# Optimization experiments

Measured on AMD Instinct MI355X. Metric: run time of the kernel, lower is better.

## Reference

```python
import jax, jax.numpy as jnp
import numpy as np

N = 50000
E = 800000
NUM_GRAPHS = 128
X_IN, HID, EDGE_DIM = 64, 64, 16


def setup_inputs() -> dict:
    key = jax.random.key(0)
    ks = jax.random.split(key, 9)
    s = 0.05
    inp = {
        'x': jax.random.normal(ks[0], (N, X_IN), jnp.float32),
        'edge_index': jax.random.randint(ks[1], (2, E), 0, N, dtype=jnp.int32),
        'edge_attr': jax.random.normal(ks[2], (E, EDGE_DIM), jnp.float32),
        'batch': jnp.sort(jax.random.randint(ks[3], (N,), 0, NUM_GRAPHS, dtype=jnp.int32)),
        'w_fc1': jax.random.normal(ks[4], (EDGE_DIM, 1), jnp.float32) * s,
        'b_fc1': jnp.zeros((1,), jnp.float32),
    }
    dims = [(X_IN, HID), (HID, HID * 2), (HID * 2, HID)]
    for i, (din, dout) in enumerate(dims):
        k1, k2, k3 = jax.random.split(ks[5 + i], 3)
        inp[f'w1_{i}'] = jax.random.normal(k1, (din, dout), jnp.float32) * s
        inp[f'b1_{i}'] = jnp.zeros((dout,), jnp.float32)
        inp[f'w2_{i}'] = jax.random.normal(k2, (din, dout), jnp.float32) * s
        inp[f'w3_{i}'] = jax.random.normal(k3, (din, dout), jnp.float32) * s
        inp[f'b3_{i}'] = jnp.zeros((dout,), jnp.float32)
    return inp


def leconv(x, src, dst, ew, w1, b1, w2, w3, b3):
    # PyG LEConv: out_i = lin3(x_i) + sum_{j->i} e_ji * (lin1(x_j) - lin2(x_i))
    a = x @ w1 + b1          # lin1 (bias=True)   [N, out]
    b = x @ w2               # lin2 (bias=False)  [N, out]
    msg = ew[:, None] * (a[src] - b[dst])          # [E, out]
    agg = jax.ops.segment_sum(msg, dst, num_segments=N)
    return agg + x @ w3 + b3  # lin3 (bias=True)


def reference(x, edge_index, edge_attr, batch,
              w_fc1, b_fc1,
              w1_0, b1_0, w2_0, w3_0, b3_0,
              w1_1, b1_1, w2_1, w3_1, b3_1,
              w1_2, b1_2, w2_2, w3_2, b3_2):
    src, dst = edge_index[0], edge_index[1]
    ew = (edge_attr @ w_fc1 + b_fc1)[:, 0]         # fc1(edge_attr).squeeze(-1) -> [E]
    h = jax.nn.elu(leconv(x, src, dst, ew, w1_0, b1_0, w2_0, w3_0, b3_0))
    h = jax.nn.elu(leconv(h, src, dst, ew, w1_1, b1_1, w2_1, w3_1, b3_1))
    h = jax.nn.elu(leconv(h, src, dst, ew, w1_2, b1_2, w2_2, w3_2, b3_2))
    # global max pool over nodes of each graph -> [NUM_GRAPHS, HID]
    return jax.ops.segment_max(h, batch, num_segments=NUM_GRAPHS)
```

## Files before the change

### kernel.cpp

```cpp
#include <hip/hip_runtime.h>
#include <math.h>

#define N_NODES 50000
#define N_EDGES 800000
#define NUM_GRAPHS_ 128
#define SCAN_NB 98
#define NPASS 8
#define NODES_PER_PASS 6250
#define HCHUNKS 128
#define EDGES_PER_CHUNK 6250
#define HWORDS 12500

typedef unsigned short u16;
typedef unsigned int u32;
typedef __attribute__((ext_vector_type(8))) short bf16x8;
typedef __attribute__((ext_vector_type(4))) float f32x4;

__device__ __forceinline__ float elu_f(float v) {
    return v > 0.f ? v : (__expf(v) - 1.f);
}
__device__ __forceinline__ u16 f2bf(float f) {
    u32 u = __float_as_uint(f);
    u += 0x7FFFu + ((u >> 16) & 1u);
    return (u16)(u >> 16);
}
__device__ __forceinline__ float bf2f(u16 h) {
    return __uint_as_float(((u32)h) << 16);
}
__device__ __forceinline__ void bfpair(u32 v, float& lo, float& hi) {
    lo = __uint_as_float(v << 16);
    hi = __uint_as_float(v & 0xFFFF0000u);
}
__device__ __forceinline__ u32 packbf(float lo, float hi) {
    return (u32)f2bf(lo) | ((u32)f2bf(hi) << 16);
}

__global__ void conv_x_kernel(const float* __restrict__ x, u16* __restrict__ xb) {
    int g = blockIdx.x * blockDim.x + threadIdx.x;
    float4 v = ((const float4*)x)[g];
    uint2 o;
    o.x = packbf(v.x, v.y);
    o.y = packbf(v.z, v.w);
    ((uint2*)xb)[g] = o;
}

__global__ void ew_kernel(const float* __restrict__ edge_attr,
                          const float* __restrict__ w_fc1,
                          const float* __restrict__ b_fc1,
                          const int* __restrict__ edge_index,
                          float* __restrict__ ew,
                          u16* __restrict__ dst16) {
    int e = blockIdx.x * blockDim.x + threadIdx.x;
    if (e >= N_EDGES) return;
    const float4* ea = (const float4*)(edge_attr + (size_t)e * 16);
    const float4* wf = (const float4*)w_fc1;
    float acc = b_fc1[0];
#pragma unroll
    for (int i = 0; i < 4; i++) {
        float4 a = ea[i], w = wf[i];
        acc += a.x * w.x + a.y * w.y + a.z * w.z + a.w * w.w;
    }
    ew[e] = acc;
    dst16[e] = (u16)edge_index[N_EDGES + e];
}

__global__ __launch_bounds__(256) void deg_hist_kernel(const u16* __restrict__ dst16,
                                                       u32* __restrict__ partial) {
    __shared__ u32 bins[HWORDS];
    const int c = blockIdx.x >> 1;
    const int p = blockIdx.x & 1;
    const int t = threadIdx.x;
    for (int i = t; i < HWORDS; i += 256) bins[i] = 0;
    __syncthreads();
    const int base = c * EDGES_PER_CHUNK;
    const int nlo = p * 25000;
    for (int i = t; i < EDGES_PER_CHUNK; i += 256) {
        const int b = (int)dst16[base + i] - nlo;
        if ((unsigned)b < 25000u)
            atomicAdd(&bins[b >> 1], 1u << ((b & 1) * 16));
    }
    __syncthreads();
    u32* outp = partial + (size_t)blockIdx.x * HWORDS;
    for (int i = t; i < HWORDS; i += 256) outp[i] = bins[i];
}

__global__ __launch_bounds__(256) void scan_chunks_kernel(const u32* __restrict__ partial,
                                                          u32* __restrict__ prefpack,
                                                          u32* __restrict__ degpack) {
    const int g = blockIdx.x * 256 + threadIdx.x;
    if (g >= 25000) return;
    const int p = (g >= HWORDS) ? 1 : 0;
    const int wh = g - p * HWORDS;
    u32 runlo = 0, runhi = 0;
    for (int c = 0; c < HCHUNKS; c++) {
        prefpack[(size_t)c * 25000 + g] = runlo | (runhi << 16);
        u32 v = partial[(size_t)((c << 1) + p) * HWORDS + wh];
        runlo += v & 0xFFFFu;
        runhi += v >> 16;
    }
    degpack[g] = runlo | (runhi << 16);
}

__global__ __launch_bounds__(256) void scan1_kernel(const u32* __restrict__ degpack,
                                                    int* __restrict__ rowptr,
                                                    int* __restrict__ blk_sums) {
    __shared__ int sh[256];
    const int t = threadIdx.x;
    const int base = blockIdx.x * 512;
    const int i0 = base + 2 * t, i1 = i0 + 1;
    int d0 = 0, d1 = 0;
    if (i0 < N_NODES) {
        u32 v = degpack[i0 >> 1];
        d0 = (int)(v & 0xFFFFu);
        d1 = (int)(v >> 16);
    }
    const int pair = d0 + d1;
    int v = pair;
    sh[t] = v;
    __syncthreads();
#pragma unroll
    for (int off = 1; off < 256; off <<= 1) {
        int add = (t >= off) ? sh[t - off] : 0;
        __syncthreads();
        v += add;
        sh[t] = v;
        __syncthreads();
    }
    const int excl = v - pair;
    if (i0 < N_NODES) rowptr[i0] = excl;
    if (i1 < N_NODES) rowptr[i1] = excl + d0;
    if (t == 255) blk_sums[blockIdx.x] = v;
}

__global__ __launch_bounds__(128) void scan2_kernel(const int* __restrict__ blk_sums,
                                                    int* __restrict__ blk_offs,
                                                    int* __restrict__ rowptr) {
    __shared__ int sh[128];
    const int t = threadIdx.x;
    const int orig = (t < SCAN_NB) ? blk_sums[t] : 0;
    int v = orig;
    sh[t] = v;
    __syncthreads();
#pragma unroll
    for (int off = 1; off < 128; off <<= 1) {
        int add = (t >= off) ? sh[t - off] : 0;
        __syncthreads();
        v += add;
        sh[t] = v;
        __syncthreads();
    }
    if (t < SCAN_NB) blk_offs[t] = v - orig;
    if (t == 127) rowptr[N_NODES] = v;
}

__global__ void scan3_kernel(int* __restrict__ rowptr,
                             const int* __restrict__ blk_offs) {
    int i = blockIdx.x * blockDim.x + threadIdx.x;
    if (i >= N_NODES) return;
    rowptr[i] += blk_offs[i >> 9];
}

__global__ __launch_bounds__(256) void place_kernel(const int* __restrict__ edge_index,
                                                    const float* __restrict__ ew,
                                                    const u16* __restrict__ dst16,
                                                    const int* __restrict__ rowptr,
                                                    const u32* __restrict__ prefpack,
                                                    int2* __restrict__ csr) {
    __shared__ int lcur[NODES_PER_PASS];
    const int pass = blockIdx.x & (NPASS - 1);
    const int c = blockIdx.x >> 3;
    const int lo = pass * NODES_PER_PASS;
    const int t = threadIdx.x;
    for (int i = t; i < NODES_PER_PASS; i += 256) lcur[i] = 0;
    __syncthreads();
    const int base = c * EDGES_PER_CHUNK;
    for (int i = t; i < EDGES_PER_CHUNK; i += 256) {
        const int e = base + i;
        const int d = (int)dst16[e];
        const int dl = d - lo;
        if ((unsigned)dl < (unsigned)NODES_PER_PASS) {
            u32 pw = prefpack[(size_t)c * 25000 + (d >> 1)];
            int pref = (int)((pw >> ((d & 1) * 16)) & 0xFFFFu);
            int lpos = atomicAdd(&lcur[dl], 1);
            int2 ent;
            ent.x = edge_index[e];
            ent.y = __float_as_int(ew[e]);
            csr[rowptr[d] + pref + lpos] = ent;
        }
    }
}

template <int DIN, bool WRITE_C>
__global__ __launch_bounds__(256) void gather_kernel(
    const u16* __restrict__ xb, const int* __restrict__ rowptr,
    const int2* __restrict__ csr, u16* __restrict__ sb,
    u16* __restrict__ chb, float* __restrict__ c) {
    constexpr int CG = DIN / 4;
    constexpr int EG = 64 / CG;
    const int gid = blockIdx.x * 256 + threadIdx.x;
    const int node = gid >> 6;
    if (node >= N_NODES) return;
    const int lane = threadIdx.x & 63;
    const int cg = lane & (CG - 1);
    const int eg = lane / CG;
    const int beg = rowptr[node];
    const int end = rowptr[node + 1];
    const uint2* x2 = (const uint2*)xb;

    float a0 = 0.f, a1 = 0.f, a2 = 0.f, a3 = 0.f;
    float b0 = 0.f, b1 = 0.f, b2 = 0.f, b3 = 0.f;
    float wsum = 0.f;

    int p = beg + eg;
    for (; p + EG < end; p += 2 * EG) {
        int2 e0 = csr[p];
        int2 e1 = csr[p + EG];
        float w0 = __int_as_float(e0.y);
        float w1 = __int_as_float(e1.y);
        uint2 v0 = x2[(size_t)e0.x * CG + cg];
        uint2 v1 = x2[(size_t)e1.x * CG + cg];
        float f0, f1, f2, f3, g0, g1, g2, g3;
        bfpair(v0.x, f0, f1); bfpair(v0.y, f2, f3);
        bfpair(v1.x, g0, g1); bfpair(v1.y, g2, g3);
        a0 += w0 * f0; a1 += w0 * f1; a2 += w0 * f2; a3 += w0 * f3;
        b0 += w1 * g0; b1 += w1 * g1; b2 += w1 * g2; b3 += w1 * g3;
        wsum += w0 + w1;
    }
    if (p < end) {
        int2 e0 = csr[p];
        float w0 = __int_as_float(e0.y);
        uint2 v0 = x2[(size_t)e0.x * CG + cg];
        float f0, f1, f2, f3;
        bfpair(v0.x, f0, f1); bfpair(v0.y, f2, f3);
        a0 += w0 * f0; a1 += w0 * f1; a2 += w0 * f2; a3 += w0 * f3;
        wsum += w0;
    }
    a0 += b0; a1 += b1; a2 += b2; a3 += b3;

#pragma unroll
    for (int off = 32; off >= CG; off >>= 1) {
        a0 += __shfl_xor(a0, off);
        a1 += __shfl_xor(a1, off);
        a2 += __shfl_xor(a2, off);
        a3 += __shfl_xor(a3, off);
        wsum += __shfl_xor(wsum, off);
    }

    if (lane < CG) {
        uint2 so;
        so.x = packbf(a0, a1);
        so.y = packbf(a2, a3);
        ((uint2*)sb)[(size_t)node * CG + cg] = so;
        const float cn = WRITE_C ? wsum : c[node];
        uint2 hv = x2[(size_t)node * CG + cg];
        float h0, h1, h2, h3;
        bfpair(hv.x, h0, h1); bfpair(hv.y, h2, h3);
        uint2 co;
        co.x = packbf(cn * h0, cn * h1);
        co.y = packbf(cn * h2, cn * h3);
        ((uint2*)chb)[(size_t)node * CG + cg] = co;
    }
    if (WRITE_C && lane == 0) c[node] = wsum;
}

__global__ void pack_w_kernel(const float* __restrict__ w3_0, const float* __restrict__ w1_0, const float* __restrict__ w2_0,
                              const float* __restrict__ w3_1, const float* __restrict__ w1_1, const float* __restrict__ w2_1,
                              const float* __restrict__ w3_2, const float* __restrict__ w1_2, const float* __restrict__ w2_2,
                              u16* __restrict__ bp0, u16* __restrict__ bp1, u16* __restrict__ bp2) {
    int t = blockIdx.x * blockDim.x + threadIdx.x;
    if (t >= 7680) return;
    u16 buf[8];
    if (t < 4608) {
        int DIN, DOUT, lid;
        const float *w3, *w1, *w2;
        u16* bp;
        if (t < 1536) { DIN = 64; DOUT = 64;  lid = t;        w3 = w3_0; w1 = w1_0; w2 = w2_0; bp = bp0; }
        else          { DIN = 64; DOUT = 128; lid = t - 1536; w3 = w3_1; w1 = w1_1; w2 = w2_1; bp = bp1; }
        const int NT = DOUT / 16;
        const int lane = lid & 63;
        const int fragid = lid >> 6;
        const int chunk = fragid / NT;
        const int ntile = fragid % NT;
        const int n = ntile * 16 + (lane & 15);
        const int kbase = chunk * 32 + (lane >> 4) * 8;
#pragma unroll
        for (int j = 0; j < 8; j++) {
            int k = kbase + j;
            int region = k / DIN;
            int kk = k - region * DIN;
            float v = (region == 0) ? w3[kk * DOUT + n]
                    : (region == 1) ? w1[kk * DOUT + n]
                                    : -w2[kk * DOUT + n];
            buf[j] = f2bf(v);
        }
        *(bf16x8*)(bp + ((size_t)lid << 3)) = *(bf16x8*)buf;
    } else {
        const int lid = t - 4608;
        const int NT = 12;
        const int lane = lid & 63;
        const int fragid = lid >> 6;
        const int chunk = fragid / NT;
        const int ntile = fragid % NT;
        const int n = ntile * 16 + (lane & 15);
        const int kbase = chunk * 32 + (lane >> 4) * 8;
#pragma unroll
        for (int j = 0; j < 8; j++) {
            int k = kbase + j;
            float v = (n < 64)  ? w3_2[k * 64 + n]
                    : (n < 128) ? -w2_2[k * 64 + (n - 64)]
                                : w1_2[k * 64 + (n - 128)];
            buf[j] = f2bf(v);
        }
        *(bf16x8*)(bp2 + ((size_t)lid << 3)) = *(bf16x8*)buf;
    }
}

template <int DIN, int DOUT>
__global__ __launch_bounds__(256) void gemm_mfma(
    const u16* __restrict__ hb, const u16* __restrict__ sb,
    const u16* __restrict__ chb, const u16* __restrict__ Bp,
    const float* __restrict__ cvec, const float* __restrict__ bias1,
    const float* __restrict__ bias3, u16* __restrict__ outp) {
    constexpr int CH = DIN / 32;
    constexpr int CHUNKS = 3 * CH;
    constexpr int NT = DOUT / 16;
    const int tid = threadIdx.x;
    const int wv = tid >> 6;
    const int lane = tid & 63;
    const int l15 = lane & 15;
    const int q = lane >> 4;
    const int mhalf = wv & 1;
    const int nhalf = wv >> 1;
    const int row_base = blockIdx.x * 64 + mhalf * 32;
    const int nt0 = blockIdx.y * 4 + nhalf * 2;

    const int r0 = min(row_base + l15, N_NODES - 1);
    const int r1 = min(row_base + 16 + l15, N_NODES - 1);
    const int qo = q * 8;

    f32x4 acc00 = {0.f, 0.f, 0.f, 0.f};
    f32x4 acc01 = {0.f, 0.f, 0.f, 0.f};
    f32x4 acc10 = {0.f, 0.f, 0.f, 0.f};
    f32x4 acc11 = {0.f, 0.f, 0.f, 0.f};

#pragma unroll
    for (int chunk = 0; chunk < CHUNKS; chunk++) {
        const int region = chunk / CH;
        const int koff = (chunk - region * CH) * 32 + qo;
        const u16* A = (region == 0) ? hb : (region == 1) ? sb : chb;
        bf16x8 a0 = *(const bf16x8*)(A + (size_t)r0 * DIN + koff);
        bf16x8 a1 = *(const bf16x8*)(A + (size_t)r1 * DIN + koff);
        const u16* bp = Bp + (((size_t)(chunk * NT + nt0) * 64 + lane) << 3);
        bf16x8 bf0 = *(const bf16x8*)bp;
        bf16x8 bf1 = *(const bf16x8*)(bp + 64 * 8);
        acc00 = __builtin_amdgcn_mfma_f32_16x16x32_bf16(a0, bf0, acc00, 0, 0, 0);
        acc01 = __builtin_amdgcn_mfma_f32_16x16x32_bf16(a0, bf1, acc01, 0, 0, 0);
        acc10 = __builtin_amdgcn_mfma_f32_16x16x32_bf16(a1, bf0, acc10, 0, 0, 0);
        acc11 = __builtin_amdgcn_mfma_f32_16x16x32_bf16(a1, bf1, acc11, 0, 0, 0);
    }

#pragma unroll
    for (int ni = 0; ni < 2; ni++) {
        const int col = (nt0 + ni) * 16 + l15;
        const float B3 = bias3[col];
        const float B1 = bias1[col];
        const f32x4 am0 = ni ? acc01 : acc00;
        const f32x4 am1 = ni ? acc11 : acc10;
#pragma unroll
        for (int mi = 0; mi < 2; mi++) {
            const f32x4 av = mi ? am1 : am0;
#pragma unroll
            for (int reg = 0; reg < 4; reg++) {
                const int row = row_base + mi * 16 + q * 4 + reg;
                if (row < N_NODES) {
                    const float cv = cvec[row];
                    const float val = av[reg] + B3 + cv * B1;
                    outp[(size_t)row * DOUT + col] = f2bf(elu_f(val));
                }
            }
        }
    }
}

__global__ __launch_bounds__(256) void gemm_wide_kernel(
    const u16* __restrict__ hb, const u16* __restrict__ Bp,
    u16* __restrict__ zuy) {
    constexpr int NT = 12;
    const int tid = threadIdx.x;
    const int wv = tid >> 6;
    const int lane = tid & 63;
    const int l15 = lane & 15;
    const int q = lane >> 4;
    const int row_base = blockIdx.x * 64 + (wv & 1) * 32;
    const int nt0 = blockIdx.y * 4 + (wv >> 1) * 2;

    const int r0 = min(row_base + l15, N_NODES - 1);
    const int r1 = min(row_base + 16 + l15, N_NODES - 1);
    const int qo = q * 8;

    f32x4 acc00 = {0.f, 0.f, 0.f, 0.f};
    f32x4 acc01 = {0.f, 0.f, 0.f, 0.f};
    f32x4 acc10 = {0.f, 0.f, 0.f, 0.f};
    f32x4 acc11 = {0.f, 0.f, 0.f, 0.f};

#pragma unroll
    for (int chunk = 0; chunk < 4; chunk++) {
        const int koff = chunk * 32 + qo;
        bf16x8 a0 = *(const bf16x8*)(hb + (size_t)r0 * 128 + koff);
        bf16x8 a1 = *(const bf16x8*)(hb + (size_t)r1 * 128 + koff);
        const u16* bp = Bp + (((size_t)(chunk * NT + nt0) * 64 + lane) << 3);
        bf16x8 bf0 = *(const bf16x8*)bp;
        bf16x8 bf1 = *(const bf16x8*)(bp + 64 * 8);
        acc00 = __builtin_amdgcn_mfma_f32_16x16x32_bf16(a0, bf0, acc00, 0, 0, 0);
        acc01 = __builtin_amdgcn_mfma_f32_16x16x32_bf16(a0, bf1, acc01, 0, 0, 0);
        acc10 = __builtin_amdgcn_mfma_f32_16x16x32_bf16(a1, bf0, acc10, 0, 0, 0);
        acc11 = __builtin_amdgcn_mfma_f32_16x16x32_bf16(a1, bf1, acc11, 0, 0, 0);
    }

#pragma unroll
    for (int ni = 0; ni < 2; ni++) {
        const int col = (nt0 + ni) * 16 + l15;
        const f32x4 am0 = ni ? acc01 : acc00;
        const f32x4 am1 = ni ? acc11 : acc10;
#pragma unroll
        for (int mi = 0; mi < 2; mi++) {
            const f32x4 av = mi ? am1 : am0;
#pragma unroll
            for (int reg = 0; reg < 4; reg++) {
                const int row = row_base + mi * 16 + q * 4 + reg;
                if (row < N_NODES)
                    zuy[(size_t)row * 192 + col] = f2bf(av[reg]);
            }
        }
    }
}

__global__ __launch_bounds__(256) void gather2_kernel(
    const u16* __restrict__ zuy, const int* __restrict__ rowptr,
    const int2* __restrict__ csr, const float* __restrict__ c,
    const float* __restrict__ bias1, const float* __restrict__ bias3,
    u16* __restrict__ h3) {
    constexpr int CG = 16, EG = 4;
    const int gid = blockIdx.x * 256 + threadIdx.x;
    const int node = gid >> 6;
    if (node >= N_NODES) return;
    const int lane = threadIdx.x & 63;
    const int cg = lane & (CG - 1);
    const int eg = lane >> 4;
    const int beg = rowptr[node];
    const int end = rowptr[node + 1];

    float a0 = 0.f, a1 = 0.f, a2 = 0.f, a3 = 0.f;
    float b0 = 0.f, b1 = 0.f, b2 = 0.f, b3 = 0.f;

    int p = beg + eg;
    for (; p + EG < end; p += 2 * EG) {
        int2 e0 = csr[p];
        int2 e1 = csr[p + EG];
        float w0 = __int_as_float(e0.y);
        float w1 = __int_as_float(e1.y);
        uint2 v0 = ((const uint2*)(zuy + (size_t)e0.x * 192 + 128))[cg];
        uint2 v1 = ((const uint2*)(zuy + (size_t)e1.x * 192 + 128))[cg];
        float f0, f1, f2, f3, g0, g1, g2, g3;
        bfpair(v0.x, f0, f1); bfpair(v0.y, f2, f3);
        bfpair(v1.x, g0, g1); bfpair(v1.y, g2, g3);
        a0 += w0 * f0; a1 += w0 * f1; a2 += w0 * f2; a3 += w0 * f3;
        b0 += w1 * g0; b1 += w1 * g1; b2 += w1 * g2; b3 += w1 * g3;
    }
    if (p < end) {
        int2 e0 = csr[p];
        float w0 = __int_as_float(e0.y);
        uint2 v0 = ((const uint2*)(zuy + (size_t)e0.x * 192 + 128))[cg];
        float f0, f1, f2, f3;
        bfpair(v0.x, f0, f1); bfpair(v0.y, f2, f3);
        a0 += w0 * f0; a1 += w0 * f1; a2 += w0 * f2; a3 += w0 * f3;
    }
    a0 += b0; a1 += b1; a2 += b2; a3 += b3;

#pragma unroll
    for (int off = 32; off >= CG; off >>= 1) {
        a0 += __shfl_xor(a0, off);
        a1 += __shfl_xor(a1, off);
        a2 += __shfl_xor(a2, off);
        a3 += __shfl_xor(a3, off);
    }

    if (lane < CG) {
        const float cn = c[node];
        const u16* zr = zuy + (size_t)node * 192;
        uint2 zv = ((const uint2*)zr)[cg];
        uint2 uv = ((const uint2*)(zr + 64))[cg];
        float z0, z1, z2, z3, u0, u1, u2, u3;
        bfpair(zv.x, z0, z1); bfpair(zv.y, z2, z3);
        bfpair(uv.x, u0, u1); bfpair(uv.y, u2, u3);
        const float4 b3v = *(const float4*)(bias3 + cg * 4);
        const float4 b1v = *(const float4*)(bias1 + cg * 4);
        float o0 = elu_f(z0 + cn * u0 + a0 + b3v.x + cn * b1v.x);
        float o1 = elu_f(z1 + cn * u1 + a1 + b3v.y + cn * b1v.y);
        float o2 = elu_f(z2 + cn * u2 + a2 + b3v.z + cn * b1v.z);
        float o3 = elu_f(z3 + cn * u3 + a3 + b3v.w + cn * b1v.w);
        uint2 o;
        o.x = packbf(o0, o1);
        o.y = packbf(o2, o3);
        ((uint2*)h3)[(size_t)node * CG + cg] = o;
    }
}

__global__ void pool_kernel(const u16* __restrict__ h,
                            const int* __restrict__ batch,
                            float* __restrict__ out) {
    const int g = blockIdx.x;
    const int tid = threadIdx.x;
    int lo = 0, hi = N_NODES;
    while (lo < hi) { int mid = (lo + hi) >> 1; if (batch[mid] < g) lo = mid + 1; else hi = mid; }
    const int beg = lo;
    lo = beg; hi = N_NODES;
    while (lo < hi) { int mid = (lo + hi) >> 1; if (batch[mid] < g + 1) lo = mid + 1; else hi = mid; }
    const int end = lo;

    __shared__ float red[256];
    const int col = tid & 63;
    const int rg = tid >> 6;
    float m = -3.0e38f;
    for (int r = beg + rg; r < end; r += 4) m = fmaxf(m, bf2f(h[(size_t)r * 64 + col]));
    red[tid] = m;
    __syncthreads();
    if (tid < 64) {
        m = fmaxf(fmaxf(red[tid], red[tid + 64]), fmaxf(red[tid + 128], red[tid + 192]));
        out[g * 64 + tid] = m;
    }
}

extern "C" void kernel_launch(void* const* d_in, const int* in_sizes, int n_in,
                              void* d_out, int out_size, void* d_ws, size_t ws_size,
                              hipStream_t stream) {
    const float* x = (const float*)d_in[0];
    const int* ei = (const int*)d_in[1];
    const float* ea = (const float*)d_in[2];
    const int* batch = (const int*)d_in[3];
    const float* wfc = (const float*)d_in[4];
    const float* bfc = (const float*)d_in[5];
    const float* w1_0 = (const float*)d_in[6];
    const float* b1_0 = (const float*)d_in[7];
    const float* w2_0 = (const float*)d_in[8];
    const float* w3_0 = (const float*)d_in[9];
    const float* b3_0 = (const float*)d_in[10];
    const float* w1_1 = (const float*)d_in[11];
    const float* b1_1 = (const float*)d_in[12];
    const float* w2_1 = (const float*)d_in[13];
    const float* w3_1 = (const float*)d_in[14];
    const float* b3_1 = (const float*)d_in[15];
    const float* w1_2 = (const float*)d_in[16];
    const float* b1_2 = (const float*)d_in[17];
    const float* w2_2 = (const float*)d_in[18];
    const float* w3_2 = (const float*)d_in[19];
    const float* b3_2 = (const float*)d_in[20];
    float* out = (float*)d_out;

    char* ws = (char*)d_ws;
    float* ew      = (float*)(ws);
    float* c       = (float*)(ws + 3200000);
    int*   rowptr  = (int*)  (ws + 3800000);
    int2*  csr     = (int2*) (ws + 4000128);
    u16*   xb      = (u16*)  (ws + 10400128);
    u16*   sb      = (u16*)  (ws + 16800128);
    u16*   chb     = (u16*)  (ws + 29600128);
    u16*   h1      = (u16*)  (ws + 42400128);
    u16*   h2      = (u16*)  (ws + 48800128);
    u16*   h3      = (u16*)  (ws + 61600128);
    u16*   bp0     = (u16*)  (ws + 68000128);
    u16*   bp1     = (u16*)  (ws + 68024704);
    u16*   bp2     = (u16*)  (ws + 68073856);
    int* blk_sums  = (int*)  (ws + 68123008);
    int* blk_offs  = (int*)  (ws + 68123520);
    u16* dst16   = chb;
    u32* degpack = (u32*)(ws + 31600128);
    u32* partial = (u32*)sb;
    u32* prefpack = (u32*)h2;
    u16* zuy     = sb;

    conv_x_kernel<<<3125, 256, 0, stream>>>(x, xb);
    ew_kernel<<<(N_EDGES + 255) / 256, 256, 0, stream>>>(ea, wfc, bfc, ei, ew, dst16);
    pack_w_kernel<<<30, 256, 0, stream>>>(w3_0, w1_0, w2_0, w3_1, w1_1, w2_1,
                                          w3_2, w1_2, w2_2, bp0, bp1, bp2);
    deg_hist_kernel<<<HCHUNKS * 2, 256, 0, stream>>>(dst16, partial);
    scan_chunks_kernel<<<98, 256, 0, stream>>>(partial, prefpack, degpack);
    scan1_kernel<<<SCAN_NB, 256, 0, stream>>>(degpack, rowptr, blk_sums);
    scan2_kernel<<<1, 128, 0, stream>>>(blk_sums, blk_offs, rowptr);
    scan3_kernel<<<(N_NODES + 255) / 256, 256, 0, stream>>>(rowptr, blk_offs);
    place_kernel<<<HCHUNKS * NPASS, 256, 0, stream>>>(ei, ew, dst16, rowptr, prefpack, csr);

    const int RB = (N_NODES + 63) / 64;
    const int GBLK = (N_NODES * 64 + 255) / 256;

    gather_kernel<64, true><<<GBLK, 256, 0, stream>>>(xb, rowptr, csr, sb, chb, c);
    gemm_mfma<64, 64><<<dim3(RB, 1), 256, 0, stream>>>(xb, sb, chb, bp0, c, b1_0, b3_0, h1);

    gather_kernel<64, false><<<GBLK, 256, 0, stream>>>(h1, rowptr, csr, sb, chb, c);
    gemm_mfma<64, 128><<<dim3(RB, 2), 256, 0, stream>>>(h1, sb, chb, bp1, c, b1_1, b3_1, h2);

    gemm_wide_kernel<<<dim3(RB, 3), 256, 0, stream>>>(h2, bp2, zuy);
    gather2_kernel<<<GBLK, 256, 0, stream>>>(zuy, rowptr, csr, c, b1_2, b3_2, h3);

    pool_kernel<<<NUM_GRAPHS_, 256, 0, stream>>>(h3, batch, out);
}
```

Before: 349.7 us.

## Pack CSR entries to 32 bits, widen gather loads, merge prep kernels

Compresses each CSR entry from an int2 (src index, fp32 weight) to one u32 holding a 16-bit source index and a bf16 edge weight. This halves CSR traffic in the three gather passes. The gathers now use 8 lanes per row with 16-byte loads and 8 edges in flight. The x conversion, edge-weight and weight-packing kernels are fused into one launch, and histogram chunks go from 128 to 64. Rounding the edge weights to bf16 adds precision loss, and the 16-bit source index only works because N is at most 65535.

Measured after the change: 352.0 us. No clear change (+0.7%).

```diff
diff --git a/kernel.cpp b/kernel.cpp
--- a/kernel.cpp
+++ b/kernel.cpp
@@ -7,8 +7,8 @@
 #define SCAN_NB 98
 #define NPASS 8
 #define NODES_PER_PASS 6250
-#define HCHUNKS 128
-#define EDGES_PER_CHUNK 6250
+#define HCHUNKS 64
+#define EDGES_PER_CHUNK 12500
 #define HWORDS 12500
 
 typedef unsigned short u16;
@@ -34,34 +34,88 @@
 __device__ __forceinline__ u32 packbf(float lo, float hi) {
     return (u32)f2bf(lo) | ((u32)f2bf(hi) << 16);
 }
-
-__global__ void conv_x_kernel(const float* __restrict__ x, u16* __restrict__ xb) {
-    int g = blockIdx.x * blockDim.x + threadIdx.x;
-    float4 v = ((const float4*)x)[g];
-    uint2 o;
-    o.x = packbf(v.x, v.y);
-    o.y = packbf(v.z, v.w);
-    ((uint2*)xb)[g] = o;
-}
-
-__global__ void ew_kernel(const float* __restrict__ edge_attr,
-                          const float* __restrict__ w_fc1,
-                          const float* __restrict__ b_fc1,
-                          const int* __restrict__ edge_index,
-                          float* __restrict__ ew,
-                          u16* __restrict__ dst16) {
-    int e = blockIdx.x * blockDim.x + threadIdx.x;
-    if (e >= N_EDGES) return;
-    const float4* ea = (const float4*)(edge_attr + (size_t)e * 16);
-    const float4* wf = (const float4*)w_fc1;
-    float acc = b_fc1[0];
-#pragma unroll
-    for (int i = 0; i < 4; i++) {
-        float4 a = ea[i], w = wf[i];
-        acc += a.x * w.x + a.y * w.y + a.z * w.z + a.w * w.w;
-    }
-    ew[e] = acc;
-    dst16[e] = (u16)edge_index[N_EDGES + e];
+__device__ __forceinline__ void unpack8(uint4 v, float* f) {
+    bfpair(v.x, f[0], f[1]); bfpair(v.y, f[2], f[3]);
+    bfpair(v.z, f[4], f[5]); bfpair(v.w, f[6], f[7]);
+}
+
+__global__ __launch_bounds__(256) void prep_kernel(
+    const float* __restrict__ x, u16* __restrict__ xb,
+    const float* __restrict__ edge_attr, const float* __restrict__ w_fc1,
+    const float* __restrict__ b_fc1, const int* __restrict__ edge_index,
+    float* __restrict__ ew, u16* __restrict__ dst16,
+    const float* __restrict__ w3_0, const float* __restrict__ w1_0, const float* __restrict__ w2_0,
+    const float* __restrict__ w3_1, const float* __restrict__ w1_1, const float* __restrict__ w2_1,
+    const float* __restrict__ w3_2, const float* __restrict__ w1_2, const float* __restrict__ w2_2,
+    u16* __restrict__ bp0, u16* __restrict__ bp1, u16* __restrict__ bp2) {
+    const int b = blockIdx.x;
+    if (b < 3125) {
+        int g = b * 256 + threadIdx.x;
+        float4 v = ((const float4*)x)[g];
+        uint2 o;
+        o.x = packbf(v.x, v.y);
+        o.y = packbf(v.z, v.w);
+        ((uint2*)xb)[g] = o;
+    } else if (b < 6250) {
+        int e = (b - 3125) * 256 + threadIdx.x;
+        const float4* ea = (const float4*)(edge_attr + (size_t)e * 16);
+        const float4* wf = (const float4*)w_fc1;
+        float acc = b_fc1[0];
+#pragma unroll
+        for (int i = 0; i < 4; i++) {
+            float4 a = ea[i], w = wf[i];
+            acc += a.x * w.x + a.y * w.y + a.z * w.z + a.w * w.w;
+        }
+        ew[e] = acc;
+        dst16[e] = (u16)edge_index[N_EDGES + e];
+    } else {
+        int t = (b - 6250) * 256 + threadIdx.x;
+        if (t >= 7680) return;
+        u16 buf[8];
+        if (t < 4608) {
+            int DIN, DOUT, lid;
+            const float *w3, *w1, *w2;
+            u16* bp;
+            if (t < 1536) { DIN = 64; DOUT = 64;  lid = t;        w3 = w3_0; w1 = w1_0; w2 = w2_0; bp = bp0; }
+            else          { DIN = 64; DOUT = 128; lid = t - 1536; w3 = w3_1; w1 = w1_1; w2 = w2_1; bp = bp1; }
+            const int NT = DOUT / 16;
+            const int lane = lid & 63;
+            const int fragid = lid >> 6;
+            const int chunk = fragid / NT;
+            const int ntile = fragid % NT;
+            const int n = ntile * 16 + (lane & 15);
+            const int kbase = chunk * 32 + (lane >> 4) * 8;
+#pragma unroll
+            for (int j = 0; j < 8; j++) {
+                int k = kbase + j;
+                int region = k / DIN;
+                int kk = k - region * DIN;
+                float v = (region == 0) ? w3[kk * DOUT + n]
+                        : (region == 1) ? w1[kk * DOUT + n]
+                                        : -w2[kk * DOUT + n];
+                buf[j] = f2bf(v);
+            }
+            *(bf16x8*)(bp + ((size_t)lid << 3)) = *(bf16x8*)buf;
+        } else {
+            const int lid = t - 4608;
+            const int NT = 12;
+            const int lane = lid & 63;
+            const int fragid = lid >> 6;
+            const int chunk = fragid / NT;
+            const int ntile = fragid % NT;
+            const int n = ntile * 16 + (lane & 15);
+            const int kbase = chunk * 32 + (lane >> 4) * 8;
+#pragma unroll
+            for (int j = 0; j < 8; j++) {
+                int k = kbase + j;
+                float v = (n < 64)  ? w3_2[k * 64 + n]
+                        : (n < 128) ? -w2_2[k * 64 + (n - 64)]
+                                    : w1_2[k * 64 + (n - 128)];
+                buf[j] = f2bf(v);
+            }
+            *(bf16x8*)(bp2 + ((size_t)lid << 3)) = *(bf16x8*)buf;
+        }
+    }
 }
 
 __global__ __launch_bounds__(256) void deg_hist_kernel(const u16* __restrict__ dst16,
@@ -165,7 +219,7 @@
                                                     const u16* __restrict__ dst16,
                                                     const int* __restrict__ rowptr,
                                                     const u32* __restrict__ prefpack,
-                                                    int2* __restrict__ csr) {
+                                                    u32* __restrict__ csr) {
     __shared__ int lcur[NODES_PER_PASS];
     const int pass = blockIdx.x & (NPASS - 1);
     const int c = blockIdx.x >> 3;
@@ -182,137 +236,85 @@
             u32 pw = prefpack[(size_t)c * 25000 + (d >> 1)];
             int pref = (int)((pw >> ((d & 1) * 16)) & 0xFFFFu);
             int lpos = atomicAdd(&lcur[dl], 1);
-            int2 ent;
-            ent.x = edge_index[e];
-            ent.y = __float_as_int(ew[e]);
+            u32 ent = (u32)(u16)edge_index[e] | ((u32)f2bf(ew[e]) << 16);
             csr[rowptr[d] + pref + lpos] = ent;
         }
     }
 }
 
-template <int DIN, bool WRITE_C>
+template <bool WRITE_C>
 __global__ __launch_bounds__(256) void gather_kernel(
     const u16* __restrict__ xb, const int* __restrict__ rowptr,
-    const int2* __restrict__ csr, u16* __restrict__ sb,
+    const u32* __restrict__ csr, u16* __restrict__ sb,
     u16* __restrict__ chb, float* __restrict__ c) {
-    constexpr int CG = DIN / 4;
-    constexpr int EG = 64 / CG;
+    constexpr int CG = 8, EG = 8;
     const int gid = blockIdx.x * 256 + threadIdx.x;
     const int node = gid >> 6;
     if (node >= N_NODES) return;
     const int lane = threadIdx.x & 63;
     const int cg = lane & (CG - 1);
-    const int eg = lane / CG;
+    const int eg = lane >> 3;
     const int beg = rowptr[node];
     const int end = rowptr[node + 1];
-    const uint2* x2 = (const uint2*)xb;
-
-    float a0 = 0.f, a1 = 0.f, a2 = 0.f, a3 = 0.f;
-    float b0 = 0.f, b1 = 0.f, b2 = 0.f, b3 = 0.f;
+    const uint4* x4 = (const uint4*)xb;
+
+    float a[8] = {}, b[8] = {};
     float wsum = 0.f;
 
     int p = beg + eg;
     for (; p + EG < end; p += 2 * EG) {
-        int2 e0 = csr[p];
-        int2 e1 = csr[p + EG];
-        float w0 = __int_as_float(e0.y);
-        float w1 = __int_as_float(e1.y);
-        uint2 v0 = x2[(size_t)e0.x * CG + cg];
-        uint2 v1 = x2[(size_t)e1.x * CG + cg];
-        float f0, f1, f2, f3, g0, g1, g2, g3;
-        bfpair(v0.x, f0, f1); bfpair(v0.y, f2, f3);
-        bfpair(v1.x, g0, g1); bfpair(v1.y, g2, g3);
-        a0 += w0 * f0; a1 += w0 * f1; a2 += w0 * f2; a3 += w0 * f3;
-        b0 += w1 * g0; b1 += w1 * g1; b2 += w1 * g2; b3 += w1 * g3;
+        u32 e0 = csr[p];
+        u32 e1 = csr[p + EG];
+        float w0 = bf2f((u16)(e0 >> 16));
+        float w1 = bf2f((u16)(e1 >> 16));
+        uint4 v0 = x4[(size_t)(e0 & 0xFFFFu) * CG + cg];
+        uint4 v1 = x4[(size_t)(e1 & 0xFFFFu) * CG + cg];
+        float f[8], g[8];
+        unpack8(v0, f);
+        unpack8(v1, g);
+#pragma unroll
+        for (int j = 0; j < 8; j++) { a[j] += w0 * f[j]; b[j] += w1 * g[j]; }
         wsum += w0 + w1;
     }
     if (p < end) {
-        int2 e0 = csr[p];
-        float w0 = __int_as_float(e0.y);
-        uint2 v0 = x2[(size_t)e0.x * CG + cg];
-        float f0, f1, f2, f3;
-        bfpair(v0.x, f0, f1); bfpair(v0.y, f2, f3);
-        a0 += w0 * f0; a1 += w0 * f1; a2 += w0 * f2; a3 += w0 * f3;
+        u32 e0 = csr[p];
+        float w0 = bf2f((u16)(e0 >> 16));
+        uint4 v0 = x4[(size_t)(e0 & 0xFFFFu) * CG + cg];
+        float f[8];
+        unpack8(v0, f);
+#pragma unroll
+        for (int j = 0; j < 8; j++) a[j] += w0 * f[j];
         wsum += w0;
     }
-    a0 += b0; a1 += b1; a2 += b2; a3 += b3;
+#pragma unroll
+    for (int j = 0; j < 8; j++) a[j] += b[j];
 
 #pragma unroll
     for (int off = 32; off >= CG; off >>= 1) {
-        a0 += __shfl_xor(a0, off);
-        a1 += __shfl_xor(a1, off);
-        a2 += __shfl_xor(a2, off);
-        a3 += __shfl_xor(a3, off);
+#pragma unroll
+        for (int j = 0; j < 8; j++) a[j] += __shfl_xor(a[j], off);
         wsum += __shfl_xor(wsum, off);
     }
 
     if (lane < CG) {
-        uint2 so;
-        so.x = packbf(a0, a1);
-        so.y = packbf(a2, a3);
-        ((uint2*)sb)[(size_t)node * CG + cg] = so;
+        uint4 so;
+        so.x = packbf(a[0], a[1]);
+        so.y = packbf(a[2], a[3]);
+        so.z = packbf(a[4], a[5]);
+        so.w = packbf(a[6], a[7]);
+        ((uint4*)sb)[(size_t)node * CG + cg] = so;
         const float cn = WRITE_C ? wsum : c[node];
-        uint2 hv = x2[(size_t)node * CG + cg];
-        float h0, h1, h2, h3;
-        bfpair(hv.x, h0, h1); bfpair(hv.y, h2, h3);
-        uint2 co;
-        co.x = packbf(cn * h0, cn * h1);
-        co.y = packbf(cn * h2, cn * h3);
-        ((uint2*)chb)[(size_t)node * CG + cg] = co;
+        uint4 hv = x4[(size_t)node * CG + cg];
+        float h[8];
+        unpack8(hv, h);
+        uint4 co;
+        co.x = packbf(cn * h[0], cn * h[1]);
+        co.y = packbf(cn * h[2], cn * h[3]);
+        co.z = packbf(cn * h[4], cn * h[5]);
+        co.w = packbf(cn * h[6], cn * h[7]);
+        ((uint4*)chb)[(size_t)node * CG + cg] = co;
     }
     if (WRITE_C && lane == 0) c[node] = wsum;
-}
-
-__global__ void pack_w_kernel(const float* __restrict__ w3_0, const float* __restrict__ w1_0, const float* __restrict__ w2_0,
-                              const float* __restrict__ w3_1, const float* __restrict__ w1_1, const float* __restrict__ w2_1,
-                              const float* __restrict__ w3_2, const float* __restrict__ w1_2, const float* __restrict__ w2_2,
-                              u16* __restrict__ bp0, u16* __restrict__ bp1, u16* __restrict__ bp2) {
-    int t = blockIdx.x * blockDim.x + threadIdx.x;
-    if (t >= 7680) return;
-    u16 buf[8];
-    if (t < 4608) {
-        int DIN, DOUT, lid;
-        const float *w3, *w1, *w2;
-        u16* bp;
-        if (t < 1536) { DIN = 64; DOUT = 64;  lid = t;        w3 = w3_0; w1 = w1_0; w2 = w2_0; bp = bp0; }
-        else          { DIN = 64; DOUT = 128; lid = t - 1536; w3 = w3_1; w1 = w1_1; w2 = w2_1; bp = bp1; }
-        const int NT = DOUT / 16;
-        const int lane = lid & 63;
-        const int fragid = lid >> 6;
-        const int chunk = fragid / NT;
-        const int ntile = fragid % NT;
-        const int n = ntile * 16 + (lane & 15);
-        const int kbase = chunk * 32 + (lane >> 4) * 8;
-#pragma unroll
-        for (int j = 0; j < 8; j++) {
-            int k = kbase + j;
-            int region = k / DIN;
-            int kk = k - region * DIN;
-            float v = (region == 0) ? w3[kk * DOUT + n]
-                    : (region == 1) ? w1[kk * DOUT + n]
-                                    : -w2[kk * DOUT + n];
-            buf[j] = f2bf(v);
-        }
-        *(bf16x8*)(bp + ((size_t)lid << 3)) = *(bf16x8*)buf;
-    } else {
-        const int lid = t - 4608;
-        const int NT = 12;
-        const int lane = lid & 63;
-        const int fragid = lid >> 6;
-        const int chunk = fragid / NT;
-        const int ntile = fragid % NT;
-        const int n = ntile * 16 + (lane & 15);
-        const int kbase = chunk * 32 + (lane >> 4) * 8;
-#pragma unroll
-        for (int j = 0; j < 8; j++) {
-            int k = kbase + j;
-            float v = (n < 64)  ? w3_2[k * 64 + n]
-                    : (n < 128) ? -w2_2[k * 64 + (n - 64)]
-                                : w1_2[k * 64 + (n - 128)];
-            buf[j] = f2bf(v);
-        }
-        *(bf16x8*)(bp2 + ((size_t)lid << 3)) = *(bf16x8*)buf;
-    }
 }
 
 template <int DIN, int DOUT>
@@ -329,10 +331,8 @@
     const int lane = tid & 63;
     const int l15 = lane & 15;
     const int q = lane >> 4;
-    const int mhalf = wv & 1;
-    const int nhalf = wv >> 1;
-    const int row_base = blockIdx.x * 64 + mhalf * 32;
-    const int nt0 = blockIdx.y * 4 + nhalf * 2;
+    const int row_base = blockIdx.x * 64 + (wv & 1) * 32;
+    const int nt0 = blockIdx.y * 4 + (wv >> 1) * 2;
 
     const int r0 = min(row_base + l15, N_NODES - 1);
     const int r1 = min(row_base + 16 + l15, N_NODES - 1);
@@ -437,72 +437,77 @@
 
 __global__ __launch_bounds__(256) void gather2_kernel(
     const u16* __restrict__ zuy, const int* __restrict__ rowptr,
-    const int2* __restrict__ csr, const float* __restrict__ c,
+    const u32* __restrict__ csr, const float* __restrict__ c,
     const float* __restrict__ bias1, const float* __restrict__ bias3,
     u16* __restrict__ h3) {
-    constexpr int CG = 16, EG = 4;
+    constexpr int CG = 8, EG = 8;
     const int gid = blockIdx.x * 256 + threadIdx.x;
     const int node = gid >> 6;
     if (node >= N_NODES) return;
     const int lane = threadIdx.x & 63;
     const int cg = lane & (CG - 1);
-    const int eg = lane >> 4;
+    const int eg = lane >> 3;
     const int beg = rowptr[node];
     const int end = rowptr[node + 1];
 
-    float a0 = 0.f, a1 = 0.f, a2 = 0.f, a3 = 0.f;
-    float b0 = 0.f, b1 = 0.f, b2 = 0.f, b3 = 0.f;
+    float a[8] = {}, b[8] = {};
 
     int p = beg + eg;
     for (; p + EG < end; p += 2 * EG) {
-        int2 e0 = csr[p];
-        int2 e1 = csr[p + EG];
-        float w0 = __int_as_float(e0.y);
-        float w1 = __int_as_float(e1.y);
-        uint2 v0 = ((const uint2*)(zuy + (size_t)e0.x * 192 + 128))[cg];
-        uint2 v1 = ((const uint2*)(zuy + (size_t)e1.x * 192 + 128))[cg];
-        float f0, f1, f2, f3, g0, g1, g2, g3;
-        bfpair(v0.x, f0, f1); bfpair(v0.y, f2, f3);
-        bfpair(v1.x, g0, g1); bfpair(v1.y, g2, g3);
-        a0 += w0 * f0; a1 += w0 * f1; a2 += w0 * f2; a3 += w0 * f3;
-        b0 += w1 * g0; b1 += w1 * g1; b2 += w1 * g2; b3 += w1 * g3;
+        u32 e0 = csr[p];
+        u32 e1 = csr[p + EG];
+        float w0 = bf2f((u16)(e0 >> 16));
+        float w1 = bf2f((u16)(e1 >> 16));
+        uint4 v0 = ((const uint4*)(zuy + (size_t)(e0 & 0xFFFFu) * 192 + 128))[cg];
+        uint4 v1 = ((const uint4*)(zuy + (size_t)(e1 & 0xFFFFu) * 192 + 128))[cg];
+        float f[8], g[8];
+        unpack8(v0, f);
+        unpack8(v1, g);
+#pragma unroll
+        for (int j = 0; j < 8; j++) { a[j] += w0 * f[j]; b[j] += w1 * g[j]; }
     }
     if (p < end) {
-        int2 e0 = csr[p];
-        float w0 = __int_as_float(e0.y);
-        uint2 v0 = ((const uint2*)(zuy + (size_t)e0.x * 192 + 128))[cg];
-        float f0, f1, f2, f3;
-        bfpair(v0.x, f0, f1); bfpair(v0.y, f2, f3);
-        a0 += w0 * f0; a1 += w0 * f1; a2 += w0 * f2; a3 += w0 * f3;
-    }
-    a0 += b0; a1 += b1; a2 += b2; a3 += b3;
+        u32 e0 = csr[p];
+        float w0 = bf2f((u16)(e0 >> 16));
+        uint4 v0 = ((const uint4*)(zuy + (size_t)(e0 & 0xFFFFu) * 192 + 128))[cg];
+        float f[8];
+        unpack8(v0, f);
+#pragma unroll
+        for (int j = 0; j < 8; j++) a[j] += w0 * f[j];
+    }
+#pragma unroll
+    for (int j = 0; j < 8; j++) a[j] += b[j];
 
 #pragma unroll
     for (int off = 32; off >= CG; off >>= 1) {
-        a0 += __shfl_xor(a0, off);
-        a1 += __shfl_xor(a1, off);
-        a2 += __shfl_xor(a2, off);
-        a3 += __shfl_xor(a3, off);
+#pragma unroll
+        for (int j = 0; j < 8; j++) a[j] += __shfl_xor(a[j], off);
     }
 
     if (lane < CG) {
         const float cn = c[node];
         const u16* zr = zuy + (size_t)node * 192;
-        uint2 zv = ((const uint2*)zr)[cg];
-        uint2 uv = ((const uint2*)(zr + 64))[cg];
-        float z0, z1, z2, z3, u0, u1, u2, u3;
-        bfpair(zv.x, z0, z1); bfpair(zv.y, z2, z3);
-        bfpair(uv.x, u0, u1); bfpair(uv.y, u2, u3);
-        const float4 b3v = *(const float4*)(bias3 + cg * 4);
-        const float4 b1v = *(const float4*)(bias1 + cg * 4);
-        float o0 = elu_f(z0 + cn * u0 + a0 + b3v.x + cn * b1v.x);
-        float o1 = elu_f(z1 + cn * u1 + a1 + b3v.y + cn * b1v.y);
-        float o2 = elu_f(z2 + cn * u2 + a2 + b3v.z + cn * b1v.z);
-        float o3 = elu_f(z3 + cn * u3 + a3 + b3v.w + cn * b1v.w);
-        uint2 o;
-        o.x = packbf(o0, o1);
-        o.y = packbf(o2, o3);
-        ((uint2*)h3)[(size_t)node * CG + cg] = o;
+        uint4 zv = ((const uint4*)zr)[cg];
+        uint4 uv = ((const uint4*)(zr + 64))[cg];
+        float z[8], u[8];
+        unpack8(zv, z);
+        unpack8(uv, u);
+        const float4 b3a = *(const float4*)(bias3 + cg * 8);
+        const float4 b3b = *(const float4*)(bias3 + cg * 8 + 4);
+        const float4 b1a = *(const float4*)(bias1 + cg * 8);
+        const float4 b1b = *(const float4*)(bias1 + cg * 8 + 4);
+        float b3v[8] = {b3a.x, b3a.y, b3a.z, b3a.w, b3b.x, b3b.y, b3b.z, b3b.w};
+        float b1v[8] = {b1a.x, b1a.y, b1a.z, b1a.w, b1b.x, b1b.y, b1b.z, b1b.w};
+        float o[8];
+#pragma unroll
+        for (int j = 0; j < 8; j++)
+            o[j] = elu_f(z[j] + cn * u[j] + a[j] + b3v[j] + cn * b1v[j]);
+        uint4 ov;
+        ov.x = packbf(o[0], o[1]);
+        ov.y = packbf(o[2], o[3]);
+        ov.z = packbf(o[4], o[5]);
+        ov.w = packbf(o[6], o[7]);
+        ((uint4*)h3)[(size_t)node * CG + cg] = ov;
     }
 }
 
@@ -561,7 +566,7 @@
     float* ew      = (float*)(ws);
     float* c       = (float*)(ws + 3200000);
     int*   rowptr  = (int*)  (ws + 3800000);
-    int2*  csr     = (int2*) (ws + 4000128);
+    u32*   csr     = (u32*)  (ws + 4000128);
     u16*   xb      = (u16*)  (ws + 10400128);
     u16*   sb      = (u16*)  (ws + 16800128);
     u16*   chb     = (u16*)  (ws + 29600128);
@@ -579,9 +584,8 @@
     u32* prefpack = (u32*)h2;
     u16* zuy     = sb;
 
-    conv_x_kernel<<<3125, 256, 0, stream>>>(x, xb);
-    ew_kernel<<<(N_EDGES + 255) / 256, 256, 0, stream>>>(ea, wfc, bfc, ei, ew, dst16);
-    pack_w_kernel<<<30, 256, 0, stream>>>(w3_0, w1_0, w2_0, w3_1, w1_1, w2_1,
+    prep_kernel<<<6280, 256, 0, stream>>>(x, xb, ea, wfc, bfc, ei, ew, dst16,
+                                          w3_0, w1_0, w2_0, w3_1, w1_1, w2_1,
                                           w3_2, w1_2, w2_2, bp0, bp1, bp2);
     deg_hist_kernel<<<HCHUNKS * 2, 256, 0, stream>>>(dst16, partial);
     scan_chunks_kernel<<<98, 256, 0, stream>>>(partial, prefpack, degpack);
@@ -593,10 +597,10 @@
     const int RB = (N_NODES + 63) / 64;
     const int GBLK = (N_NODES * 64 + 255) / 256;
 
-    gather_kernel<64, true><<<GBLK, 256, 0, stream>>>(xb, rowptr, csr, sb, chb, c);
+    gather_kernel<true><<<GBLK, 256, 0, stream>>>(xb, rowptr, csr, sb, chb, c);
     gemm_mfma<64, 64><<<dim3(RB, 1), 256, 0, stream>>>(xb, sb, chb, bp0, c, b1_0, b3_0, h1);
 
-    gather_kernel<64, false><<<GBLK, 256, 0, stream>>>(h1, rowptr, csr, sb, chb, c);
+    gather_kernel<false><<<GBLK, 256, 0, stream>>>(h1, rowptr, csr, sb, chb, c);
     gemm_mfma<64, 128><<<dim3(RB, 2), 256, 0, stream>>>(h1, sb, chb, bp1, c, b1_1, b3_1, h2);
 
     gemm_wide_kernel<<<dim3(RB, 3), 256, 0, stream>>>(h2, bp2, zuy);
```
